# Optimization experiments

Hardware: AMD Instinct MI355X
Metric: run time of the kernel (lower is better)

The kernel has to match this reference:

```python
import jax, jax.numpy as jnp
import numpy as np
from jax import lax

D_MODEL = 256
N_LAYERS = 4
D_STATE = 64
EXPAND = 2
HEADDIM = 64
D_CONV = 4
D_INNER = EXPAND * D_MODEL                      # 512
NHEADS = D_INNER // HEADDIM                     # 8
CONV_DIM = D_INNER + 2 * D_STATE                # 640 (ngroups=1)
D_IN_PROJ = 2 * D_INNER + 2 * D_STATE + NHEADS  # 1160
B_SZ, SEQ = 8, 2048


def _silu(x):
    return x * jax.nn.sigmoid(x)


def _mamba2(u, W_in, W_conv, b_conv, dt_bias, A_log, Dp, norm_w, W_out):
    # Standard Mamba2 block (in_proj -> causal depthwise conv -> selective scan
    # with per-head scalar A -> gated RMSNorm -> out_proj).
    B, L, _ = u.shape
    zxbcdt = u @ W_in.T                                   # [B,L,1160]
    z = zxbcdt[..., :D_INNER]
    xBC = zxbcdt[..., D_INNER:D_INNER + CONV_DIM]
    dt = jax.nn.softplus(zxbcdt[..., D_INNER + CONV_DIM:] + dt_bias)  # [B,L,H]
    # causal depthwise conv1d + silu
    xc = lax.conv_general_dilated(xBC.transpose(0, 2, 1), W_conv[:, None, :],
                                  (1,), [(D_CONV - 1, 0)],
                                  dimension_numbers=('NCH', 'OIH', 'NCH'),
                                  feature_group_count=CONV_DIM)
    xBC = _silu(xc.transpose(0, 2, 1) + b_conv)
    x = xBC[..., :D_INNER].reshape(B, L, NHEADS, HEADDIM)
    Bm = xBC[..., D_INNER:D_INNER + D_STATE]              # [B,L,N]
    Cm = xBC[..., D_INNER + D_STATE:]                     # [B,L,N]
    dA = jnp.exp(dt * (-jnp.exp(A_log)))                  # [B,L,H]

    def step(h, inp):
        dA_t, dt_t, x_t, B_t, C_t = inp
        # h: [B,H,P,N]
        h = dA_t[:, :, None, None] * h + (dt_t[:, :, None] * x_t)[..., None] * B_t[:, None, None, :]
        y = jnp.einsum('bhpn,bn->bhp', h, C_t)
        return h, y

    h0 = jnp.zeros((B, NHEADS, HEADDIM, D_STATE), u.dtype)
    xs = (dA.transpose(1, 0, 2), dt.transpose(1, 0, 2), x.transpose(1, 0, 2, 3),
          Bm.transpose(1, 0, 2), Cm.transpose(1, 0, 2))
    _, ys = lax.scan(step, h0, xs)                        # [L,B,H,P]
    y = ys.transpose(1, 0, 2, 3) + Dp[None, None, :, None] * x
    y = y.reshape(B, L, D_INNER)
    y = y * _silu(z)                                      # gate before RMSNorm
    y = y * lax.rsqrt(jnp.mean(y * y, axis=-1, keepdims=True) + 1e-5) * norm_w
    return y @ W_out.T


def _encoder(x, pf, pb):
    for i in range(N_LAYERS - 1):
        y_fwd = _mamba2(x, *[p[i] for p in pf])
        y_bwd = _mamba2(x[:, ::-1], *[p[i] for p in pb])[:, ::-1]
        x = y_fwd + y_bwd
    h_fwd = _mamba2(x, *[p[-1] for p in pf])
    h_bwd = _mamba2(x[:, ::-1], *[p[-1] for p in pb])[:, ::-1]
    H = (h_fwd + h_bwd).mean(axis=1)
    return h_fwd, h_bwd, H


def _make_params(key):
    k = jax.random.split(key, 4)
    W_in = jax.random.normal(k[0], (N_LAYERS, D_IN_PROJ, D_MODEL), jnp.float32) * 0.02
    W_conv = jax.random.normal(k[1], (N_LAYERS, CONV_DIM, D_CONV), jnp.float32) * 0.2
    b_conv = jnp.zeros((N_LAYERS, CONV_DIM), jnp.float32)
    dt = jnp.exp(jax.random.uniform(k[2], (N_LAYERS, NHEADS)) * (np.log(0.1) - np.log(0.001)) + np.log(0.001))
    dt_bias = dt + jnp.log(-jnp.expm1(-dt))               # softplus^{-1}(dt)
    A_log = jnp.log(jax.random.uniform(k[3], (N_LAYERS, NHEADS), minval=1.0, maxval=16.0))
    Dp = jnp.ones((N_LAYERS, NHEADS), jnp.float32)
    norm_w = jnp.ones((N_LAYERS, D_INNER), jnp.float32)
    W_out = jax.random.normal(jax.random.fold_in(k[0], 7), (N_LAYERS, D_MODEL, D_INNER), jnp.float32) * 0.02
    return (W_in, W_conv, b_conv, dt_bias, A_log, Dp, norm_w, W_out)


def setup_inputs():
    key = jax.random.key(0)
    kx, kf, kb = jax.random.split(key, 3)
    x = jax.random.normal(kx, (B_SZ, SEQ, D_MODEL), jnp.float32)
    pf = _make_params(kf)
    pb = _make_params(kb)
    names = ['Win', 'Wconv', 'bconv', 'dt_bias', 'A_log', 'D', 'norm_w', 'Wout']
    inp = {'x_conditioned': x}
    for n, p in zip(names, pf):
        inp[n + '_f'] = p
    for n, p in zip(names, pb):
        inp[n + '_b'] = p
    return inp


def reference(x_conditioned, Win_f, Wconv_f, bconv_f, dt_bias_f, A_log_f, D_f, norm_w_f, Wout_f,
              Win_b, Wconv_b, bconv_b, dt_bias_b, A_log_b, D_b, norm_w_b, Wout_b):
    pf = (Win_f, Wconv_f, bconv_f, dt_bias_f, A_log_f, D_f, norm_w_f, Wout_f)
    pb = (Win_b, Wconv_b, bconv_b, dt_bias_b, A_log_b, D_b, norm_w_b, Wout_b)
    return _encoder(x_conditioned, pf, pb)
```

## Files before the change

### kernel.cpp

```cpp
#include <hip/hip_runtime.h>
#include <math.h>


#define TC 64
#define NC 32
#define SPITCH 72
#define HIOFF 8388608

typedef __attribute__((ext_vector_type(4))) float f32x4;
typedef __attribute__((ext_vector_type(8))) short s16x8;

#define MFMA __builtin_amdgcn_mfma_f32_16x16x32_bf16

__device__ __forceinline__ float siluf(float x) { return x / (1.f + expf(-x)); }

__device__ __forceinline__ ushort f2b(float f) {
  union { float f; uint u; } v; v.f = f;
  return (ushort)((v.u + 0x7FFFu + ((v.u >> 16) & 1u)) >> 16);
}
__device__ __forceinline__ float b2f(ushort u) {
  union { uint u; float f; } v; v.u = ((uint)u) << 16; return v.f;
}
__device__ __forceinline__ int swz(int r, int c) { return c ^ (r & 3) ^ ((r >> 2) & 3); }

__device__ __forceinline__ int soff(int base, int r, int cc) {
  return base + r * SPITCH + ((((cc >> 3) ^ (r & 7) ^ ((r >> 3) & 7)) << 3) | (cc & 7));
}

__device__ __forceinline__ int toff(int base, int r, int cc) {
  return base + r * 64 + ((((cc >> 3) ^ (r & 7)) << 3) | (cc & 7));
}

__device__ __forceinline__ void cvt8(const float4 v0, const float4 v1, s16x8& hh, s16x8& ll) {
  const float a[8] = {v0.x, v0.y, v0.z, v0.w, v1.x, v1.y, v1.z, v1.w};
#pragma unroll
  for (int e = 0; e < 8; ++e) {
    const ushort hb = f2b(a[e]);
    hh[e] = (short)hb;
    ll[e] = (short)f2b(a[e] - b2f(hb));
  }
}

__device__ __forceinline__ void stage16t(ushort* tiles, const float* src,
                                         int bh_, int bl_, int r, int c0) {
  const float4 v0 = *(const float4*)(src + c0);
  const float4 v1 = *(const float4*)(src + c0 + 4);
  const float4 v2 = *(const float4*)(src + c0 + 8);
  const float4 v3 = *(const float4*)(src + c0 + 12);
  s16x8 h0, l0, h1, l1;
  cvt8(v0, v1, h0, l0);
  cvt8(v2, v3, h1, l1);
  *(s16x8*)&tiles[toff(bh_, r, c0)]     = h0;
  *(s16x8*)&tiles[toff(bl_, r, c0)]     = l0;
  *(s16x8*)&tiles[toff(bh_, r, c0 + 8)] = h1;
  *(s16x8*)&tiles[toff(bl_, r, c0 + 8)] = l1;
}

__global__ __launch_bounds__(256) void k_cvt(
    const float* __restrict__ src, ushort* __restrict__ dst, int n8)
{
  const int i = blockIdx.x * 256 + threadIdx.x;
  if (i >= n8) return;
  const float4 v0 = *(const float4*)(src + (size_t)i * 8);
  const float4 v1 = *(const float4*)(src + (size_t)i * 8 + 4);
  s16x8 h;
#pragma unroll
  for (int e = 0; e < 4; ++e) h[e] = (short)f2b(((const float*)&v0)[e]);
#pragma unroll
  for (int e = 0; e < 4; ++e) h[e + 4] = (short)f2b(((const float*)&v1)[e]);
  *(s16x8*)(dst + (size_t)i * 8) = h;
}

__global__ __launch_bounds__(256) void k_gemmb(
    const ushort* __restrict__ A, int arev,
    const ushort* __restrict__ W, int N, int K,
    ushort* __restrict__ zb, ushort* __restrict__ xbc,
    const float* __restrict__ dt_bias, const float* __restrict__ A_log,
    float* __restrict__ dtb, float* __restrict__ dab)
{
  __shared__ __align__(16) ushort lds[17408];
  const int tid = threadIdx.x;
  const int lane = tid & 63;
  const int wid = tid >> 6;
  const int wr = wid >> 1, wc = wid & 1;
  const int m0 = blockIdx.x * 128, n0 = blockIdx.y * 128;

  const int tr = tid >> 1;
  const int th = tid & 1;
  const int gm = m0 + tr;
  const int bb = gm >> 11, tt = gm & 2047;
  const int tphys = arev ? (2047 - tt) : tt;
  const ushort* Arow = A + (size_t)((bb << 11) + tphys) * 256 + th * 16;
  const int wn = n0 + tr;
  const ushort* Wrow = (wn < N) ? (W + (size_t)wn * K + th * 16) : nullptr;

  const int asw0 = tr * 32 + swz(tr, th * 2) * 8;
  const int asw1 = tr * 32 + swz(tr, th * 2 + 1) * 8;

  f32x4 acc[4][4];
#pragma unroll
  for (int i = 0; i < 4; ++i)
#pragma unroll
    for (int j = 0; j < 4; ++j) acc[i][j] = (f32x4){0.f, 0.f, 0.f, 0.f};

  int aoff[4], boff[4];
#pragma unroll
  for (int f = 0; f < 4; ++f) {
    const int ar = wr * 64 + f * 16 + (lane & 15);
    aoff[f] = ar * 32 + swz(ar, lane >> 4) * 8;
    const int br = wc * 64 + f * 16 + (lane & 15);
    boff[f] = 4096 + br * 32 + swz(br, lane >> 4) * 8;
  }

  const s16x8 zz = (s16x8){0, 0, 0, 0, 0, 0, 0, 0};
  s16x8 a0 = *(const s16x8*)(Arow);
  s16x8 a1 = *(const s16x8*)(Arow + 8);
  s16x8 b0 = zz, b1 = zz;
  if (Wrow) {
    b0 = *(const s16x8*)(Wrow);
    b1 = *(const s16x8*)(Wrow + 8);
  }

  for (int k0 = 0; k0 < K; k0 += 32) {
    __syncthreads();
    *(s16x8*)&lds[asw0] = a0;
    *(s16x8*)&lds[asw1] = a1;
    *(s16x8*)&lds[4096 + asw0] = b0;
    *(s16x8*)&lds[4096 + asw1] = b1;
    __syncthreads();
    if (k0 + 32 < K) {
      a0 = *(const s16x8*)(Arow + k0 + 32);
      a1 = *(const s16x8*)(Arow + k0 + 40);
      if (Wrow) {
        b0 = *(const s16x8*)(Wrow + k0 + 32);
        b1 = *(const s16x8*)(Wrow + k0 + 40);
      }
    }
    s16x8 af[4], bf[4];
#pragma unroll
    for (int f = 0; f < 4; ++f) {
      af[f] = *(const s16x8*)&lds[aoff[f]];
      bf[f] = *(const s16x8*)&lds[boff[f]];
    }
#pragma unroll
    for (int i = 0; i < 4; ++i)
#pragma unroll
      for (int j = 0; j < 4; ++j)
        acc[i][j] = MFMA(af[i], bf[j], acc[i][j], 0, 0, 0);
  }

  const int by = blockIdx.y;
  if (by == 9) {
    if (wc == 0 && (lane & 15) < 8) {
      const int cl = lane & 15;
      const float bias = dt_bias[cl];
      const float eAl = expf(A_log[cl]);
#pragma unroll
      for (int i = 0; i < 4; ++i) {
        const int r = m0 + wr * 64 + i * 16 + (lane >> 4) * 4;
#pragma unroll
        for (int g = 0; g < 4; ++g) {
          const float v = acc[i][0][g] + bias;
          const float sp = (v > 20.f) ? v : log1pf(expf(v));
          dtb[(size_t)(r + g) * 8 + cl] = sp;
          dab[(size_t)(r + g) * 8 + cl] = sp * eAl;
        }
      }
    }
    return;
  }
  __syncthreads();
#pragma unroll
  for (int i = 0; i < 4; ++i) {
    const int r = wr * 64 + i * 16 + (lane >> 4) * 4;
#pragma unroll
    for (int j = 0; j < 4; ++j) {
      const int ccol = wc * 64 + j * 16 + (lane & 15);
#pragma unroll
      for (int g = 0; g < 4; ++g)
        lds[(r + g) * 136 + ccol] = f2b(acc[i][j][g]);
    }
  }
  __syncthreads();
  const int rr = tid >> 1, hf = tid & 1;
  const int grow = m0 + rr;
  ushort* dst; int stride, colb;
  if (by < 4) { dst = zb;  stride = 512; colb = n0; }
  else        { dst = xbc; stride = 640; colb = n0 - 512; }
  ushort* dp = dst + (size_t)grow * stride + colb + hf * 64;
  const ushort* sp = &lds[rr * 136 + hf * 64];
#pragma unroll
  for (int q = 0; q < 8; ++q)
    *(s16x8*)(dp + q * 8) = *(const s16x8*)(sp + q * 8);
}

__global__ __launch_bounds__(256) void k_gemmo(
    const ushort* __restrict__ A, int lda,
    const ushort* __restrict__ W, int N, int K,
    float* __restrict__ Cout, ushort* __restrict__ dupb,
    int crev, int accflag)
{
  __shared__ __align__(16) ushort lds[8192];
  const int tid = threadIdx.x;
  const int lane = tid & 63;
  const int wid = tid >> 6;
  const int wr = wid >> 1, wc = wid & 1;
  const int m0 = blockIdx.x * 128, n0 = blockIdx.y * 128;

  const int tr = tid >> 1;
  const int th = tid & 1;
  const int gm = m0 + tr;
  const ushort* Arow = A + (size_t)gm * lda + th * 16;
  const int wn = n0 + tr;
  const ushort* Wrow = (wn < N) ? (W + (size_t)wn * K + th * 16) : nullptr;

  const int asw0 = tr * 32 + swz(tr, th * 2) * 8;
  const int asw1 = tr * 32 + swz(tr, th * 2 + 1) * 8;

  f32x4 acc[4][4];
#pragma unroll
  for (int i = 0; i < 4; ++i)
#pragma unroll
    for (int j = 0; j < 4; ++j) acc[i][j] = (f32x4){0.f, 0.f, 0.f, 0.f};

  int aoff[4], boff[4];
#pragma unroll
  for (int f = 0; f < 4; ++f) {
    const int ar = wr * 64 + f * 16 + (lane & 15);
    aoff[f] = ar * 32 + swz(ar, lane >> 4) * 8;
    const int br = wc * 64 + f * 16 + (lane & 15);
    boff[f] = 4096 + br * 32 + swz(br, lane >> 4) * 8;
  }

  const s16x8 zz = (s16x8){0, 0, 0, 0, 0, 0, 0, 0};
  s16x8 a0 = *(const s16x8*)(Arow);
  s16x8 a1 = *(const s16x8*)(Arow + 8);
  s16x8 b0 = zz, b1 = zz;
  if (Wrow) {
    b0 = *(const s16x8*)(Wrow);
    b1 = *(const s16x8*)(Wrow + 8);
  }

  for (int k0 = 0; k0 < K; k0 += 32) {
    __syncthreads();
    *(s16x8*)&lds[asw0] = a0;
    *(s16x8*)&lds[asw1] = a1;
    *(s16x8*)&lds[4096 + asw0] = b0;
    *(s16x8*)&lds[4096 + asw1] = b1;
    __syncthreads();
    if (k0 + 32 < K) {
      a0 = *(const s16x8*)(Arow + k0 + 32);
      a1 = *(const s16x8*)(Arow + k0 + 40);
      if (Wrow) {
        b0 = *(const s16x8*)(Wrow + k0 + 32);
        b1 = *(const s16x8*)(Wrow + k0 + 40);
      }
    }
    s16x8 af[4], bf[4];
#pragma unroll
    for (int f = 0; f < 4; ++f) {
      af[f] = *(const s16x8*)&lds[aoff[f]];
      bf[f] = *(const s16x8*)&lds[boff[f]];
    }
#pragma unroll
    for (int i = 0; i < 4; ++i)
#pragma unroll
      for (int j = 0; j < 4; ++j)
        acc[i][j] = MFMA(af[i], bf[j], acc[i][j], 0, 0, 0);
  }

#pragma unroll
  for (int i = 0; i < 4; ++i) {
    const int rb = m0 + wr * 64 + i * 16 + (lane >> 4) * 4;
#pragma unroll
    for (int g = 0; g < 4; ++g) {
      const int row = rb + g;
      const int b2_ = row >> 11, t2 = row & 2047;
      const int tw = crev ? (2047 - t2) : t2;
      const size_t rbase = ((size_t)((b2_ << 11) + tw)) * 256 + n0 + wc * 64 + (lane & 15);
      float* crow = Cout + rbase;
#pragma unroll
      for (int j = 0; j < 4; ++j) {
        float v = acc[i][j][g];
        if (accflag) v += crow[j * 16];
        if (dupb) dupb[rbase + j * 16] = f2b(v);
        if (!(accflag && dupb)) crow[j * 16] = v;
      }
    }
  }
}

__global__ __launch_bounds__(256) void k_conv(
    const ushort* __restrict__ xbc, const float* __restrict__ Wc,
    const float* __restrict__ bc, float* __restrict__ xc)
{
  const int t = threadIdx.x;
  const int cg = blockIdx.x * 8 + (t & 7);
  const int c0 = cg * 8;
  const int rt0 = (blockIdx.y * 32 + (t >> 3)) * 16;

  float4 wv[8];
  const float4* wp = (const float4*)(Wc + c0 * 4);
#pragma unroll
  for (int e = 0; e < 8; ++e) wv[e] = wp[e];
  float bias[8];
#pragma unroll
  for (int e = 0; e < 8; ++e) bias[e] = bc[c0 + e];

  const s16x8 zz = (s16x8){0, 0, 0, 0, 0, 0, 0, 0};
  s16x8 w0, w1, w2;
  {
    const int l0 = rt0 & 2047;
    w0 = (l0 >= 3) ? *(const s16x8*)(xbc + (size_t)(rt0 - 3) * 640 + c0) : zz;
    w1 = (l0 >= 2) ? *(const s16x8*)(xbc + (size_t)(rt0 - 2) * 640 + c0) : zz;
    w2 = (l0 >= 1) ? *(const s16x8*)(xbc + (size_t)(rt0 - 1) * 640 + c0) : zz;
  }

#pragma unroll 4
  for (int i = 0; i < 16; ++i) {
    const int row = rt0 + i;
    const s16x8 cur = *(const s16x8*)(xbc + (size_t)row * 640 + c0);
    float acc[8];
#pragma unroll
    for (int e = 0; e < 8; ++e) {
      const float* w = (const float*)&wv[e];
      float a = bias[e];
      a = fmaf(b2f((ushort)w0[e]), w[0], a);
      a = fmaf(b2f((ushort)w1[e]), w[1], a);
      a = fmaf(b2f((ushort)w2[e]), w[2], a);
      a = fmaf(b2f((ushort)cur[e]), w[3], a);
      acc[e] = a;
    }
    float* op = xc + (size_t)row * 640 + c0;
    float4 o0, o1;
    o0.x = siluf(acc[0]); o0.y = siluf(acc[1]); o0.z = siluf(acc[2]); o0.w = siluf(acc[3]);
    o1.x = siluf(acc[4]); o1.y = siluf(acc[5]); o1.z = siluf(acc[6]); o1.w = siluf(acc[7]);
    *(float4*)op = o0; *(float4*)(op + 4) = o1;
    w0 = w1; w1 = w2; w2 = cur;
  }
}

__global__ __launch_bounds__(256) void k_scan1(
    float* __restrict__ xc, const float* __restrict__ dt,
    const float* __restrict__ dtA, const float* __restrict__ Dp,
    ushort* __restrict__ hin, float* __restrict__ Sbuf,
    float* __restrict__ PT)
{
  const int c = blockIdx.x & (NC - 1);
  const int bhi = blockIdx.x >> 5;
  const int b = bhi >> 3, h = bhi & 7;
  const int tid = threadIdx.x;
  const int lane = tid & 63;
  const int wid = tid >> 6;
  const int r0 = b * 2048 + c * TC;
  const int hbase = h * 64;
  __shared__ __align__(16) ushort tiles[24576];
  __shared__ float Ssh[64], dtsh[64], vsh[64];
  enum { PCH = 0, PCL = 4096, PBH = 8192, PBL = 12288, PXH = 16384, PXL = 20480 };

  if (tid < 64) {
    float a = dtA[(size_t)(r0 + tid) * 8 + h];
    const float d = dt[(size_t)(r0 + tid) * 8 + h];
#pragma unroll
    for (int off = 1; off < 64; off <<= 1) {
      const float t = __shfl_up(a, off);
      if (tid >= off) a += t;
    }
    const float slast = __shfl(a, 63);
    Ssh[tid] = a;
    dtsh[tid] = d;
    vsh[tid] = expf(a - slast) * d;
    Sbuf[(size_t)bhi * 2048 + c * TC + tid] = a;
    if (tid == 63) PT[bhi * NC + c] = expf(-slast);
  }
  {
    const int r = tid >> 2, c0 = (tid & 3) * 16;
    const float* rowp = xc + (size_t)(r0 + r) * 640;
    stage16t(tiles, rowp + 512, PBH, PBL, r, c0);
    stage16t(tiles, rowp + 576, PCH, PCL, r, c0);
    stage16t(tiles, rowp + hbase, PXH, PXL, r, c0);
  }
  __syncthreads();

  const int ib = wid * 16;
  const int frow = lane & 15;
  const int fkc = lane >> 4;

  const int tp = tid >> 2;
  const int tj0 = (tid & 3) * 16;
  s16x8 xtr[4], btr[4];
#pragma unroll
  for (int cc = 0; cc < 2; ++cc) {
    const int j0 = tj0 + cc * 8;
    s16x8 vh, vl, wh, wl;
#pragma unroll
    for (int e = 0; e < 8; ++e) {
      const int ax = toff(PXH, j0 + e, tp);
      vh[e] = (short)tiles[ax];
      vl[e] = (short)tiles[ax + 4096];
      const int ab = toff(PBH, j0 + e, tp);
      wh[e] = (short)tiles[ab];
      wl[e] = (short)tiles[ab + 4096];
    }
    xtr[cc] = vh; xtr[cc + 2] = vl;
    btr[cc] = wh; btr[cc + 2] = wl;
  }

  s16x8 pah[2], pal[2];
#pragma unroll
  for (int ks = 0; ks < 2; ++ks) {
    pah[ks] = *(const s16x8*)&tiles[toff(PCH, ib + frow, ks * 32 + fkc * 8)];
    pal[ks] = *(const s16x8*)&tiles[toff(PCL, ib + frow, ks * 32 + fkc * 8)];
  }
  f32x4 acc[4];
#pragma unroll
  for (int jt = 0; jt < 4; ++jt) acc[jt] = (f32x4){0.f, 0.f, 0.f, 0.f};
#pragma unroll
  for (int jt = 0; jt < 4; ++jt) {
#pragma unroll
    for (int ks = 0; ks < 2; ++ks) {
      const s16x8 tbh = *(const s16x8*)&tiles[toff(PBH, jt * 16 + frow, ks * 32 + fkc * 8)];
      const s16x8 tbl = *(const s16x8*)&tiles[toff(PBL, jt * 16 + frow, ks * 32 + fkc * 8)];
      acc[jt] = MFMA(pah[ks], tbh, acc[jt], 0, 0, 0);
      acc[jt] = MFMA(pah[ks], tbl, acc[jt], 0, 0, 0);
      acc[jt] = MFMA(pal[ks], tbh, acc[jt], 0, 0, 0);
    }
  }
  float Si[4];
#pragma unroll
  for (int g = 0; g < 4; ++g) Si[g] = Ssh[ib + fkc * 4 + g];
#pragma unroll
  for (int jt = 0; jt < 4; ++jt) {
    const int j = jt * 16 + frow;
    const float Sj = Ssh[j], dj = dtsh[j];
#pragma unroll
    for (int g = 0; g < 4; ++g) {
      const int i = ib + fkc * 4 + g;
      const float w = (j <= i) ? __expf(Sj - Si[g]) * dj : 0.f;
      const float gt = acc[jt][g] * w;
      const ushort gh = f2b(gt);
      tiles[toff(PCH, i, j)] = gh;
      tiles[toff(PCL, i, j)] = f2b(gt - b2f(gh));
    }
  }
  __syncthreads();

#pragma unroll
  for (int cc = 0; cc < 2; ++cc) {
    *(s16x8*)&tiles[toff(PXH, tp, tj0 + cc * 8)] = xtr[cc];
    *(s16x8*)&tiles[toff(PXL, tp, tj0 + cc * 8)] = xtr[cc + 2];
    *(s16x8*)&tiles[toff(PBH, tp, tj0 + cc * 8)] = btr[cc];
    *(s16x8*)&tiles[toff(PBL, tp, tj0 + cc * 8)] = btr[cc + 2];
  }
  __syncthreads();

  s16x8 gah[2], gal[2];
#pragma unroll
  for (int ks = 0; ks < 2; ++ks) {
    gah[ks] = *(const s16x8*)&tiles[toff(PCH, ib + frow, ks * 32 + fkc * 8)];
    gal[ks] = *(const s16x8*)&tiles[toff(PCL, ib + frow, ks * 32 + fkc * 8)];
  }
  const float dpv = Dp[h];
#pragma unroll
  for (int pt = 0; pt < 4; ++pt) {
    f32x4 accY = (f32x4){0.f, 0.f, 0.f, 0.f};
#pragma unroll
    for (int ks = 0; ks < 2; ++ks) {
      const s16x8 xh = *(const s16x8*)&tiles[toff(PXH, pt * 16 + frow, ks * 32 + fkc * 8)];
      const s16x8 xl = *(const s16x8*)&tiles[toff(PXL, pt * 16 + frow, ks * 32 + fkc * 8)];
      accY = MFMA(gah[ks], xh, accY, 0, 0, 0);
      accY = MFMA(gah[ks], xl, accY, 0, 0, 0);
      accY = MFMA(gal[ks], xh, accY, 0, 0, 0);
    }
    const int p = pt * 16 + frow;
#pragma unroll
    for (int g = 0; g < 4; ++g) {
      const int i = ib + fkc * 4 + g;
      float* ap = xc + (size_t)(r0 + i) * 640 + hbase + p;
      *ap = accY[g] + dpv * (*ap);
    }
  }

  s16x8 xvh[2], xvl[2];
#pragma unroll
  for (int ks = 0; ks < 2; ++ks) {
    const int J0 = ks * 32 + fkc * 8;
    const s16x8 xh = *(const s16x8*)&tiles[toff(PXH, ib + frow, J0)];
    const s16x8 xl = *(const s16x8*)&tiles[toff(PXL, ib + frow, J0)];
#pragma unroll
    for (int e = 0; e < 8; ++e) {
      const float xf = (b2f((ushort)xh[e]) + b2f((ushort)xl[e])) * vsh[J0 + e];
      const ushort nh = f2b(xf);
      xvh[ks][e] = (short)nh;
      xvl[ks][e] = (short)f2b(xf - b2f(nh));
    }
  }
  ushort* hbp = hin + (((size_t)(bhi * NC + c)) << 12);
#pragma unroll
  for (int nt = 0; nt < 4; ++nt) {
    f32x4 accC = (f32x4){0.f, 0.f, 0.f, 0.f};
#pragma unroll
    for (int ks = 0; ks < 2; ++ks) {
      const s16x8 tbh = *(const s16x8*)&tiles[toff(PBH, nt * 16 + frow, ks * 32 + fkc * 8)];
      const s16x8 tbl = *(const s16x8*)&tiles[toff(PBL, nt * 16 + frow, ks * 32 + fkc * 8)];
      accC = MFMA(xvh[ks], tbh, accC, 0, 0, 0);
      accC = MFMA(xvh[ks], tbl, accC, 0, 0, 0);
      accC = MFMA(xvl[ks], tbh, accC, 0, 0, 0);
    }
    const int n = nt * 16 + frow;
    const int kss = nt >> 1;
    const int nlo3 = (n >> 3) & 3, ne = n & 7;
#pragma unroll
    for (int g = 0; g < 4; ++g) {
      const int plo = fkc * 4 + g;
      const int off = ((wid * 2 + kss) << 9) + (nlo3 * 16 + plo) * 8 + ne;
      const float v = accC[g];
      const ushort vh = f2b(v);
      hbp[off] = vh;
      hbp[off + HIOFF] = f2b(v - b2f(vh));
    }
  }
}

__global__ __launch_bounds__(256) void k_scan2(
    ushort* __restrict__ hin, const float* __restrict__ PT)
{
  const int bh = blockIdx.x >> 2, jt = blockIdx.x & 3;
  const int t = threadIdx.x;
  float hv[4] = {0.f, 0.f, 0.f, 0.f};
  for (int c = 0; c < NC; ++c) {
    ushort* base = hin + (((size_t)(bh * NC + c)) << 12) + (jt << 10) + t * 4;
    const float pt = PT[bh * NC + c];
    const ushort4 uh = *(const ushort4*)base;
    const ushort4 ul = *(const ushort4*)(base + HIOFF);
    const float vals[4] = {b2f(uh.x) + b2f(ul.x), b2f(uh.y) + b2f(ul.y),
                           b2f(uh.z) + b2f(ul.z), b2f(uh.w) + b2f(ul.w)};
    ushort4 nh, nl;
    ushort* nhp = (ushort*)&nh; ushort* nlp = (ushort*)&nl;
#pragma unroll
    for (int k = 0; k < 4; ++k) {
      const float old = hv[k];
      hv[k] = fmaf(pt, hv[k], vals[k]);
      const ushort oh = f2b(old);
      nhp[k] = oh;
      nlp[k] = f2b(old - b2f(oh));
    }
    *(ushort4*)base = nh;
    *(ushort4*)(base + HIOFF) = nl;
  }
}

__global__ __launch_bounds__(512) void k_scan3f(
    const float* __restrict__ xc, const ushort* __restrict__ z,
    const ushort* __restrict__ hin, const float* __restrict__ Sbuf,
    const float* __restrict__ normw, ushort* __restrict__ ybf)
{
  const int c = blockIdx.x & (NC - 1);
  const int b = blockIdx.x >> 5;
  const int tid = threadIdx.x;
  const int lane = tid & 63;
  const int h = tid >> 6;
  const int r0 = b * 2048 + c * TC;
  const int frow = lane & 15;
  const int fk = (lane >> 4) * 8;
  __shared__ __align__(16) ushort ybuf[64 * 524];
  __shared__ float Esh[8][64];
  __shared__ float partial[64][9];
  __shared__ float scale[64];

  {
    const int r = tid >> 3, c0 = (tid & 7) * 8;
    const float4 v0 = *(const float4*)(xc + (size_t)(r0 + r) * 640 + 576 + c0);
    const float4 v1 = *(const float4*)(xc + (size_t)(r0 + r) * 640 + 576 + c0 + 4);
    s16x8 hh, ll;
    cvt8(v0, v1, hh, ll);
    *(s16x8*)&ybuf[soff(0, r, c0)] = hh;
    *(s16x8*)&ybuf[soff(4608, r, c0)] = ll;
  }
  Esh[h][lane] = expf(-Sbuf[(size_t)((b * 8 + h) << 11) + c * TC + lane]);
  __syncthreads();

  const size_t cbase = ((size_t)((b * 8 + h) * NC + c)) << 12;
  s16x8 Bh[4][2], Bl[4][2];
  const ushort* hb = hin + cbase + lane * 8;
#pragma unroll
  for (int jt = 0; jt < 4; ++jt)
#pragma unroll
    for (int ks = 0; ks < 2; ++ks) {
      Bh[jt][ks] = *(const s16x8*)(hb + ((jt * 2 + ks) << 9));
      Bl[jt][ks] = *(const s16x8*)(hb + ((jt * 2 + ks) << 9) + HIOFF);
    }
  s16x8 Ah[4][2], Al[4][2];
#pragma unroll
  for (int it = 0; it < 4; ++it)
#pragma unroll
    for (int ks = 0; ks < 2; ++ks) {
      Ah[it][ks] = *(const s16x8*)&ybuf[soff(0, it * 16 + frow, ks * 32 + fk)];
      Al[it][ks] = *(const s16x8*)&ybuf[soff(4608, it * 16 + frow, ks * 32 + fk)];
    }

  f32x4 acc[4][4];
#pragma unroll
  for (int it = 0; it < 4; ++it)
#pragma unroll
    for (int jt = 0; jt < 4; ++jt) acc[it][jt] = (f32x4){0.f, 0.f, 0.f, 0.f};
#pragma unroll
  for (int it = 0; it < 4; ++it)
#pragma unroll
    for (int jt = 0; jt < 4; ++jt)
#pragma unroll
      for (int ks = 0; ks < 2; ++ks) {
        acc[it][jt] = MFMA(Ah[it][ks], Bh[jt][ks], acc[it][jt], 0, 0, 0);
        acc[it][jt] = MFMA(Ah[it][ks], Bl[jt][ks], acc[it][jt], 0, 0, 0);
        acc[it][jt] = MFMA(Al[it][ks], Bh[jt][ks], acc[it][jt], 0, 0, 0);
      }

  float rowsq[4][4];
#pragma unroll
  for (int it = 0; it < 4; ++it)
#pragma unroll
    for (int g = 0; g < 4; ++g) rowsq[it][g] = 0.f;
#pragma unroll
  for (int it = 0; it < 4; ++it)
#pragma unroll
    for (int jt = 0; jt < 4; ++jt) {
      const int gcol = h * 64 + jt * 16 + frow;
#pragma unroll
      for (int g = 0; g < 4; ++g) {
        const int row = it * 16 + (lane >> 4) * 4 + g;
        const float yl = xc[(size_t)(r0 + row) * 640 + gcol];
        const float zf = b2f(z[(size_t)(r0 + row) * 512 + gcol]);
        const float y = (yl + Esh[h][row] * acc[it][jt][g]) * siluf(zf);
        acc[it][jt][g] = y;
        rowsq[it][g] = fmaf(y, y, rowsq[it][g]);
      }
    }
#pragma unroll
  for (int it = 0; it < 4; ++it)
#pragma unroll
    for (int g = 0; g < 4; ++g) {
      float s = rowsq[it][g];
      s += __shfl_xor(s, 1);
      s += __shfl_xor(s, 2);
      s += __shfl_xor(s, 4);
      s += __shfl_xor(s, 8);
      if (frow == 0) partial[it * 16 + (lane >> 4) * 4 + g][h] = s;
    }
  __syncthreads();
  if (tid < 64) {
    float s = 0.f;
#pragma unroll
    for (int hh = 0; hh < 8; ++hh) s += partial[tid][hh];
    scale[tid] = rsqrtf(s * (1.f / 512.f) + 1e-5f);
  }
  __syncthreads();

  float wreg[4];
#pragma unroll
  for (int jt = 0; jt < 4; ++jt) wreg[jt] = normw[h * 64 + jt * 16 + frow];
#pragma unroll
  for (int it = 0; it < 4; ++it)
#pragma unroll
    for (int jt = 0; jt < 4; ++jt) {
      const int col = h * 64 + jt * 16 + frow;
#pragma unroll
      for (int g = 0; g < 4; ++g) {
        const int row = it * 16 + (lane >> 4) * 4 + g;
        ybuf[row * 524 + col] = f2b(acc[it][jt][g] * scale[row] * wreg[jt]);
      }
    }
  __syncthreads();
#pragma unroll
  for (int j = 0; j < 8; ++j) {
    const int flat = j * 4096 + tid * 8;
    const int row = flat >> 9, col = flat & 511;
    const ushort4 u0 = *(const ushort4*)&ybuf[row * 524 + col];
    const ushort4 u1 = *(const ushort4*)&ybuf[row * 524 + col + 4];
    s16x8 o;
    o[0] = (short)u0.x; o[1] = (short)u0.y; o[2] = (short)u0.z; o[3] = (short)u0.w;
    o[4] = (short)u1.x; o[5] = (short)u1.y; o[6] = (short)u1.z; o[7] = (short)u1.w;
    *(s16x8*)(ybf + (size_t)(r0 + row) * 512 + col) = o;
  }
}

__global__ __launch_bounds__(256) void k_hpart(
    const float* __restrict__ hf, const float* __restrict__ hb,
    float* __restrict__ part)
{
  const int g = blockIdx.x;
  const int b = g >> 5, seg = g & 31;
  const int m = threadIdx.x;
  float s = 0.f;
  for (int l = seg * 64; l < seg * 64 + 64; ++l) {
    const size_t idx = ((size_t)b * 2048 + l) * 256 + m;
    s += hf[idx] + hb[idx];
  }
  part[(size_t)g * 256 + m] = s;
}

__global__ __launch_bounds__(256) void k_hfinal(
    const float* __restrict__ part, float* __restrict__ H)
{
  const int b = blockIdx.x;
  const int m = threadIdx.x;
  float s = 0.f;
  for (int g = 0; g < 32; ++g) s += part[(size_t)(b * 32 + g) * 256 + m];
  H[b * 256 + m] = s * (1.f / 2048.f);
}

extern "C" void kernel_launch(void* const* d_in, const int* in_sizes, int n_in,
                              void* d_out, int out_size, void* d_ws, size_t ws_size,
                              hipStream_t stream) {
  const float* x_in = (const float*)d_in[0];
  const float* Win[2]    = {(const float*)d_in[1],  (const float*)d_in[9]};
  const float* Wconv[2]  = {(const float*)d_in[2],  (const float*)d_in[10]};
  const float* bconv[2]  = {(const float*)d_in[3],  (const float*)d_in[11]};
  const float* dtbias[2] = {(const float*)d_in[4],  (const float*)d_in[12]};
  const float* Alog[2]   = {(const float*)d_in[5],  (const float*)d_in[13]};
  const float* Dpar[2]   = {(const float*)d_in[6],  (const float*)d_in[14]};
  const float* normw[2]  = {(const float*)d_in[7],  (const float*)d_in[15]};
  const float* Wout[2]   = {(const float*)d_in[8],  (const float*)d_in[16]};

  float* ws = (float*)d_ws;
  ushort* zb    = (ushort*)ws;
  ushort* xbcb  = (ushort*)(ws + 4194304);
  ushort* ybf   = xbcb;
  ushort* hinp  = (ushort*)(ws + 9437184);
  float* xc      = ws + 17825792;
  float* dtb     = ws + 28311552;
  float* dab     = ws + 28442624;
  float* Sbuf    = ws + 28573696;
  float* acc32   = ws + 28704768;
  ushort* xbf    = (ushort*)(ws + 32899072);
  float* part    = ws + 34996224;
  ushort* Winb   = (ushort*)(ws + 35061760);
  ushort* Woutb  = (ushort*)(ws + 36249600);

  float* hF = (float*)d_out;
  float* hB = hF + (size_t)8 * 2048 * 256;
  float* Hm = hB + (size_t)8 * 2048 * 256;

  k_cvt<<<580, 256, 0, stream>>>(Win[0], Winb, 148480);
  k_cvt<<<580, 256, 0, stream>>>(Win[1], Winb + 1187840, 148480);
  k_cvt<<<256, 256, 0, stream>>>(Wout[0], Woutb, 65536);
  k_cvt<<<256, 256, 0, stream>>>(Wout[1], Woutb + 524288, 65536);
  k_cvt<<<2048, 256, 0, stream>>>(x_in, xbf, 524288);

  for (int layer = 0; layer < 4; ++layer) {
    for (int dir = 0; dir < 2; ++dir) {
      const ushort* Wi = Winb + ((size_t)dir * 4 + layer) * 1160 * 256;
      const ushort* Wo = Woutb + ((size_t)dir * 4 + layer) * 256 * 512;
      const float* Wc = Wconv[dir]  + (size_t)layer * 640 * 4;
      const float* bc = bconv[dir]  + (size_t)layer * 640;
      const float* db = dtbias[dir] + (size_t)layer * 8;
      const float* Al = Alog[dir]   + (size_t)layer * 8;
      const float* Dl = Dpar[dir]   + (size_t)layer * 8;
      const float* nw = normw[dir]  + (size_t)layer * 512;

      k_gemmb<<<dim3(128, 10), 256, 0, stream>>>(xbf, dir, Wi, 1160, 256,
                                                 zb, xbcb, db, Al, dtb, dab);
      k_conv<<<dim3(10, 32), 256, 0, stream>>>(xbcb, Wc, bc, xc);
      k_scan1<<<2048, 256, 0, stream>>>(xc, dtb, dab, Dl, hinp, Sbuf, part);
      k_scan2<<<256, 256, 0, stream>>>(hinp, part);
      k_scan3f<<<256, 512, 0, stream>>>(xc, zb, hinp, Sbuf, nw, ybf);

      float* outp; ushort* dupb; int accf;
      if (layer < 3) {
        outp = acc32; accf = dir;
        dupb = dir ? xbf : nullptr;
      } else {
        outp = dir ? hB : hF; accf = 0; dupb = nullptr;
      }
      k_gemmo<<<dim3(128, 2), 256, 0, stream>>>(ybf, 512, Wo, 256, 512,
                                                outp, dupb, dir, accf);
    }
  }
  k_hpart<<<256, 256, 0, stream>>>(hF, hB, part);
  k_hfinal<<<8, 256, 0, stream>>>(part, Hm);
}
```

Baseline: 1.203 ms.

## Batch forward and backward directions into single launches via grid z dimension

Runs both scan directions concurrently by adding a z grid dimension to every per-layer kernel, with duplicated workspace buffers for each direction. This halves the number of kernel launches and doubles per-launch parallelism, which helps the small scan2/scan3/conv grids fill the GPU. The mid-layer output projection now accumulates both directions' GEMMs inside one kernel and writes the bf16 sum directly, removing the fp32 intermediate accumulation buffer round-trip. It needs roughly twice the workspace memory.

After: 1.019 ms. -15.3%, faster.

```diff
diff --git a/kernel.cpp b/kernel.cpp
--- a/kernel.cpp
+++ b/kernel.cpp
@@ -7,6 +7,14 @@
 #define SPITCH 72
 #define HIOFF 8388608
 
+#define ZB_STR   8388608u
+#define XBCB_STR 10485760u
+#define HINP_STR 16777216u
+#define XC_STR   10485760u
+#define DT_STR   131072u
+#define SB_STR   131072u
+#define PT_STR   2048u
+
 typedef __attribute__((ext_vector_type(4))) float f32x4;
 typedef __attribute__((ext_vector_type(8))) short s16x8;
 
@@ -26,7 +34,6 @@
 __device__ __forceinline__ int soff(int base, int r, int cc) {
   return base + r * SPITCH + ((((cc >> 3) ^ (r & 7) ^ ((r >> 3) & 7)) << 3) | (cc & 7));
 }
-
 __device__ __forceinline__ int toff(int base, int r, int cc) {
   return base + r * 64 + ((((cc >> 3) ^ (r & 7)) << 3) | (cc & 7));
 }
@@ -72,12 +79,22 @@
 }
 
 __global__ __launch_bounds__(256) void k_gemmb(
-    const ushort* __restrict__ A, int arev,
-    const ushort* __restrict__ W, int N, int K,
+    const ushort* __restrict__ A, const ushort* __restrict__ Winb, int layer,
     ushort* __restrict__ zb, ushort* __restrict__ xbc,
-    const float* __restrict__ dt_bias, const float* __restrict__ A_log,
+    const float* __restrict__ db0, const float* __restrict__ db1,
+    const float* __restrict__ Al0, const float* __restrict__ Al1,
     float* __restrict__ dtb, float* __restrict__ dab)
 {
+  const int zd = blockIdx.z;
+  const ushort* W = Winb + ((size_t)zd * 4 + layer) * 296960;
+  zb  += (size_t)zd * ZB_STR;
+  xbc += (size_t)zd * XBCB_STR;
+  dtb += (size_t)zd * DT_STR;
+  dab += (size_t)zd * DT_STR;
+  const float* dt_bias = zd ? db1 : db0;
+  const float* A_log   = zd ? Al1 : Al0;
+  const int N = 1160, K = 256;
+
   __shared__ __align__(16) ushort lds[17408];
   const int tid = threadIdx.x;
   const int lane = tid & 63;
@@ -89,7 +106,7 @@
   const int th = tid & 1;
   const int gm = m0 + tr;
   const int bb = gm >> 11, tt = gm & 2047;
-  const int tphys = arev ? (2047 - tt) : tt;
+  const int tphys = zd ? (2047 - tt) : tt;
   const ushort* Arow = A + (size_t)((bb << 11) + tphys) * 256 + th * 16;
   const int wn = n0 + tr;
   const ushort* Wrow = (wn < N) ? (W + (size_t)wn * K + th * 16) : nullptr;
@@ -194,11 +211,9 @@
     *(s16x8*)(dp + q * 8) = *(const s16x8*)(sp + q * 8);
 }
 
-__global__ __launch_bounds__(256) void k_gemmo(
-    const ushort* __restrict__ A, int lda,
-    const ushort* __restrict__ W, int N, int K,
-    float* __restrict__ Cout, ushort* __restrict__ dupb,
-    int crev, int accflag)
+__global__ __launch_bounds__(256) void k_gemmo_mid(
+    const ushort* __restrict__ ybf, const ushort* __restrict__ Woutb, int layer,
+    ushort* __restrict__ xbf)
 {
   __shared__ __align__(16) ushort lds[8192];
   const int tid = threadIdx.x;
@@ -210,9 +225,8 @@
   const int tr = tid >> 1;
   const int th = tid & 1;
   const int gm = m0 + tr;
-  const ushort* Arow = A + (size_t)gm * lda + th * 16;
+  const int bb = gm >> 11, tt = gm & 2047;
   const int wn = n0 + tr;
-  const ushort* Wrow = (wn < N) ? (W + (size_t)wn * K + th * 16) : nullptr;
 
   const int asw0 = tr * 32 + swz(tr, th * 2) * 8;
   const int asw1 = tr * 32 + swz(tr, th * 2 + 1) * 8;
@@ -232,29 +246,114 @@
     boff[f] = 4096 + br * 32 + swz(br, lane >> 4) * 8;
   }
 
-  const s16x8 zz = (s16x8){0, 0, 0, 0, 0, 0, 0, 0};
+  for (int dir = 0; dir < 2; ++dir) {
+    const int tphys = dir ? (2047 - tt) : tt;
+    const ushort* Arow = ybf + (size_t)dir * ZB_STR
+                       + (size_t)((bb << 11) + tphys) * 512 + th * 16;
+    const ushort* Wrow = Woutb + ((size_t)dir * 4 + layer) * 131072
+                       + (size_t)wn * 512 + th * 16;
+    s16x8 a0 = *(const s16x8*)(Arow);
+    s16x8 a1 = *(const s16x8*)(Arow + 8);
+    s16x8 b0 = *(const s16x8*)(Wrow);
+    s16x8 b1 = *(const s16x8*)(Wrow + 8);
+    for (int k0 = 0; k0 < 512; k0 += 32) {
+      __syncthreads();
+      *(s16x8*)&lds[asw0] = a0;
+      *(s16x8*)&lds[asw1] = a1;
+      *(s16x8*)&lds[4096 + asw0] = b0;
+      *(s16x8*)&lds[4096 + asw1] = b1;
+      __syncthreads();
+      if (k0 + 32 < 512) {
+        a0 = *(const s16x8*)(Arow + k0 + 32);
+        a1 = *(const s16x8*)(Arow + k0 + 40);
+        b0 = *(const s16x8*)(Wrow + k0 + 32);
+        b1 = *(const s16x8*)(Wrow + k0 + 40);
+      }
+      s16x8 af[4], bf[4];
+#pragma unroll
+      for (int f = 0; f < 4; ++f) {
+        af[f] = *(const s16x8*)&lds[aoff[f]];
+        bf[f] = *(const s16x8*)&lds[boff[f]];
+      }
+#pragma unroll
+      for (int i = 0; i < 4; ++i)
+#pragma unroll
+        for (int j = 0; j < 4; ++j)
+          acc[i][j] = MFMA(af[i], bf[j], acc[i][j], 0, 0, 0);
+    }
+  }
+
+#pragma unroll
+  for (int i = 0; i < 4; ++i) {
+    const int rb = m0 + wr * 64 + i * 16 + (lane >> 4) * 4;
+#pragma unroll
+    for (int g = 0; g < 4; ++g) {
+      const size_t rbase = (size_t)(rb + g) * 256 + n0 + wc * 64 + (lane & 15);
+#pragma unroll
+      for (int j = 0; j < 4; ++j)
+        xbf[rbase + j * 16] = f2b(acc[i][j][g]);
+    }
+  }
+}
+
+__global__ __launch_bounds__(256) void k_gemmo_last(
+    const ushort* __restrict__ ybf, const ushort* __restrict__ Woutb,
+    float* __restrict__ hF, float* __restrict__ hB)
+{
+  const int zd = blockIdx.z;
+  const ushort* A = ybf + (size_t)zd * ZB_STR;
+  const ushort* W = Woutb + ((size_t)zd * 4 + 3) * 131072;
+  float* Cout = zd ? hB : hF;
+
+  __shared__ __align__(16) ushort lds[8192];
+  const int tid = threadIdx.x;
+  const int lane = tid & 63;
+  const int wid = tid >> 6;
+  const int wr = wid >> 1, wc = wid & 1;
+  const int m0 = blockIdx.x * 128, n0 = blockIdx.y * 128;
+
+  const int tr = tid >> 1;
+  const int th = tid & 1;
+  const int gm = m0 + tr;
+  const ushort* Arow = A + (size_t)gm * 512 + th * 16;
+  const int wn = n0 + tr;
+  const ushort* Wrow = W + (size_t)wn * 512 + th * 16;
+
+  const int asw0 = tr * 32 + swz(tr, th * 2) * 8;
+  const int asw1 = tr * 32 + swz(tr, th * 2 + 1) * 8;
+
+  f32x4 acc[4][4];
+#pragma unroll
+  for (int i = 0; i < 4; ++i)
+#pragma unroll
+    for (int j = 0; j < 4; ++j) acc[i][j] = (f32x4){0.f, 0.f, 0.f, 0.f};
+
+  int aoff[4], boff[4];
+#pragma unroll
+  for (int f = 0; f < 4; ++f) {
+    const int ar = wr * 64 + f * 16 + (lane & 15);
+    aoff[f] = ar * 32 + swz(ar, lane >> 4) * 8;
+    const int br = wc * 64 + f * 16 + (lane & 15);
+    boff[f] = 4096 + br * 32 + swz(br, lane >> 4) * 8;
+  }
+
   s16x8 a0 = *(const s16x8*)(Arow);
   s16x8 a1 = *(const s16x8*)(Arow + 8);
-  s16x8 b0 = zz, b1 = zz;
-  if (Wrow) {
-    b0 = *(const s16x8*)(Wrow);
-    b1 = *(const s16x8*)(Wrow + 8);
-  }
-
-  for (int k0 = 0; k0 < K; k0 += 32) {
+  s16x8 b0 = *(const s16x8*)(Wrow);
+  s16x8 b1 = *(const s16x8*)(Wrow + 8);
+
+  for (int k0 = 0; k0 < 512; k0 += 32) {
     __syncthreads();
     *(s16x8*)&lds[asw0] = a0;
     *(s16x8*)&lds[asw1] = a1;
     *(s16x8*)&lds[4096 + asw0] = b0;
     *(s16x8*)&lds[4096 + asw1] = b1;
     __syncthreads();
-    if (k0 + 32 < K) {
+    if (k0 + 32 < 512) {
       a0 = *(const s16x8*)(Arow + k0 + 32);
       a1 = *(const s16x8*)(Arow + k0 + 40);
-      if (Wrow) {
-        b0 = *(const s16x8*)(Wrow + k0 + 32);
-        b1 = *(const s16x8*)(Wrow + k0 + 40);
-      }
+      b0 = *(const s16x8*)(Wrow + k0 + 32);
+      b1 = *(const s16x8*)(Wrow + k0 + 40);
     }
     s16x8 af[4], bf[4];
 #pragma unroll
@@ -276,24 +375,27 @@
     for (int g = 0; g < 4; ++g) {
       const int row = rb + g;
       const int b2_ = row >> 11, t2 = row & 2047;
-      const int tw = crev ? (2047 - t2) : t2;
-      const size_t rbase = ((size_t)((b2_ << 11) + tw)) * 256 + n0 + wc * 64 + (lane & 15);
-      float* crow = Cout + rbase;
-#pragma unroll
-      for (int j = 0; j < 4; ++j) {
-        float v = acc[i][j][g];
-        if (accflag) v += crow[j * 16];
-        if (dupb) dupb[rbase + j * 16] = f2b(v);
-        if (!(accflag && dupb)) crow[j * 16] = v;
-      }
+      const int tw = zd ? (2047 - t2) : t2;
+      float* crow = Cout + ((size_t)((b2_ << 11) + tw)) * 256 + n0 + wc * 64 + (lane & 15);
+#pragma unroll
+      for (int j = 0; j < 4; ++j)
+        crow[j * 16] = acc[i][j][g];
     }
   }
 }
 
 __global__ __launch_bounds__(256) void k_conv(
-    const ushort* __restrict__ xbc, const float* __restrict__ Wc,
-    const float* __restrict__ bc, float* __restrict__ xc)
-{
+    const ushort* __restrict__ xbc,
+    const float* __restrict__ Wc0, const float* __restrict__ Wc1,
+    const float* __restrict__ bc0, const float* __restrict__ bc1,
+    float* __restrict__ xc)
+{
+  const int zd = blockIdx.z;
+  xbc += (size_t)zd * XBCB_STR;
+  xc  += (size_t)zd * XC_STR;
+  const float* Wc = zd ? Wc1 : Wc0;
+  const float* bc = zd ? bc1 : bc0;
+
   const int t = threadIdx.x;
   const int cg = blockIdx.x * 8 + (t & 7);
   const int c0 = cg * 8;
@@ -342,10 +444,20 @@
 
 __global__ __launch_bounds__(256) void k_scan1(
     float* __restrict__ xc, const float* __restrict__ dt,
-    const float* __restrict__ dtA, const float* __restrict__ Dp,
+    const float* __restrict__ dtA,
+    const float* __restrict__ Dp0, const float* __restrict__ Dp1,
     ushort* __restrict__ hin, float* __restrict__ Sbuf,
     float* __restrict__ PT)
 {
+  const int zd = blockIdx.z;
+  xc   += (size_t)zd * XC_STR;
+  dt   += (size_t)zd * DT_STR;
+  dtA  += (size_t)zd * DT_STR;
+  hin  += (size_t)zd * HINP_STR;
+  Sbuf += (size_t)zd * SB_STR;
+  PT   += (size_t)zd * PT_STR;
+  const float* Dp = zd ? Dp1 : Dp0;
+
   const int c = blockIdx.x & (NC - 1);
   const int bhi = blockIdx.x >> 5;
   const int b = bhi >> 3, h = bhi & 7;
@@ -525,6 +637,9 @@
 __global__ __launch_bounds__(256) void k_scan2(
     ushort* __restrict__ hin, const float* __restrict__ PT)
 {
+  const int zd = blockIdx.z;
+  hin += (size_t)zd * HINP_STR;
+  PT  += (size_t)zd * PT_STR;
   const int bh = blockIdx.x >> 2, jt = blockIdx.x & 3;
   const int t = threadIdx.x;
   float hv[4] = {0.f, 0.f, 0.f, 0.f};
@@ -553,8 +668,17 @@
 __global__ __launch_bounds__(512) void k_scan3f(
     const float* __restrict__ xc, const ushort* __restrict__ z,
     const ushort* __restrict__ hin, const float* __restrict__ Sbuf,
-    const float* __restrict__ normw, ushort* __restrict__ ybf)
-{
+    const float* __restrict__ nw0, const float* __restrict__ nw1,
+    ushort* __restrict__ ybf)
+{
+  const int zd = blockIdx.z;
+  xc   += (size_t)zd * XC_STR;
+  z    += (size_t)zd * ZB_STR;
+  hin  += (size_t)zd * HINP_STR;
+  Sbuf += (size_t)zd * SB_STR;
+  ybf  += (size_t)zd * ZB_STR;
+  const float* normw = zd ? nw1 : nw0;
+
   const int c = blockIdx.x & (NC - 1);
   const int b = blockIdx.x >> 5;
   const int tid = threadIdx.x;
@@ -723,18 +847,18 @@
 
   float* ws = (float*)d_ws;
   ushort* zb    = (ushort*)ws;
-  ushort* xbcb  = (ushort*)(ws + 4194304);
-  ushort* ybf   = xbcb;
-  ushort* hinp  = (ushort*)(ws + 9437184);
-  float* xc      = ws + 17825792;
-  float* dtb     = ws + 28311552;
-  float* dab     = ws + 28442624;
-  float* Sbuf    = ws + 28573696;
-  float* acc32   = ws + 28704768;
-  ushort* xbf    = (ushort*)(ws + 32899072);
-  float* part    = ws + 34996224;
-  ushort* Winb   = (ushort*)(ws + 35061760);
-  ushort* Woutb  = (ushort*)(ws + 36249600);
+  ushort* ybf   = zb;
+  ushort* xbcb  = (ushort*)(ws + 8388608);
+  ushort* hinp  = (ushort*)(ws + 18874368);
+  float* xc      = ws + 35651584;
+  float* dtb     = ws + 56623104;
+  float* dab     = ws + 56885248;
+  float* Sbuf    = ws + 57147392;
+  float* PT      = ws + 57409536;
+  float* part    = ws + 57413632;
+  ushort* xbf    = (ushort*)(ws + 57479168);
+  ushort* Winb   = (ushort*)(ws + 59576320);
+  ushort* Woutb  = (ushort*)(ws + 60764160);
 
   float* hF = (float*)d_out;
   float* hB = hF + (size_t)8 * 2048 * 256;
@@ -747,32 +871,27 @@
   k_cvt<<<2048, 256, 0, stream>>>(x_in, xbf, 524288);
 
   for (int layer = 0; layer < 4; ++layer) {
-    for (int dir = 0; dir < 2; ++dir) {
-      const ushort* Wi = Winb + ((size_t)dir * 4 + layer) * 1160 * 256;
-      const ushort* Wo = Woutb + ((size_t)dir * 4 + layer) * 256 * 512;
-      const float* Wc = Wconv[dir]  + (size_t)layer * 640 * 4;
-      const float* bc = bconv[dir]  + (size_t)layer * 640;
-      const float* db = dtbias[dir] + (size_t)layer * 8;
-      const float* Al = Alog[dir]   + (size_t)layer * 8;
-      const float* Dl = Dpar[dir]   + (size_t)layer * 8;
-      const float* nw = normw[dir]  + (size_t)layer * 512;
-
-      k_gemmb<<<dim3(128, 10), 256, 0, stream>>>(xbf, dir, Wi, 1160, 256,
-                                                 zb, xbcb, db, Al, dtb, dab);
-      k_conv<<<dim3(10, 32), 256, 0, stream>>>(xbcb, Wc, bc, xc);
-      k_scan1<<<2048, 256, 0, stream>>>(xc, dtb, dab, Dl, hinp, Sbuf, part);
-      k_scan2<<<256, 256, 0, stream>>>(hinp, part);
-      k_scan3f<<<256, 512, 0, stream>>>(xc, zb, hinp, Sbuf, nw, ybf);
-
-      float* outp; ushort* dupb; int accf;
-      if (layer < 3) {
-        outp = acc32; accf = dir;
-        dupb = dir ? xbf : nullptr;
-      } else {
-        outp = dir ? hB : hF; accf = 0; dupb = nullptr;
-      }
-      k_gemmo<<<dim3(128, 2), 256, 0, stream>>>(ybf, 512, Wo, 256, 512,
-                                                outp, dupb, dir, accf);
+    const float* Wc0 = Wconv[0] + (size_t)layer * 640 * 4;
+    const float* Wc1 = Wconv[1] + (size_t)layer * 640 * 4;
+    const float* bc0 = bconv[0] + (size_t)layer * 640;
+    const float* bc1 = bconv[1] + (size_t)layer * 640;
+
+    k_gemmb<<<dim3(128, 10, 2), 256, 0, stream>>>(
+        xbf, Winb, layer, zb, xbcb,
+        dtbias[0] + layer * 8, dtbias[1] + layer * 8,
+        Alog[0] + layer * 8, Alog[1] + layer * 8, dtb, dab);
+    k_conv<<<dim3(10, 32, 2), 256, 0, stream>>>(xbcb, Wc0, Wc1, bc0, bc1, xc);
+    k_scan1<<<dim3(2048, 1, 2), 256, 0, stream>>>(
+        xc, dtb, dab, Dpar[0] + layer * 8, Dpar[1] + layer * 8,
+        hinp, Sbuf, PT);
+    k_scan2<<<dim3(256, 1, 2), 256, 0, stream>>>(hinp, PT);
+    k_scan3f<<<dim3(256, 1, 2), 512, 0, stream>>>(
+        xc, zb, hinp, Sbuf,
+        normw[0] + layer * 512, normw[1] + layer * 512, ybf);
+    if (layer < 3) {
+      k_gemmo_mid<<<dim3(128, 2), 256, 0, stream>>>(ybf, Woutb, layer, xbf);
+    } else {
+      k_gemmo_last<<<dim3(128, 2, 2), 256, 0, stream>>>(ybf, Woutb, hF, hB);
     }
   }
   k_hpart<<<256, 256, 0, stream>>>(hF, hB, part);
```
